# Kernel tuning notes

Hardware: AMD Instinct MI355X
Metric: run time of the kernel (lower is better)

## Reference

```python
import jax, jax.numpy as jnp
import numpy as np

B, DIM = 4096, 768
HEADS, DIM_HEAD = 8, 96
INNER = HEADS * DIM_HEAD  # 768
N_IDS = 751


def setup_inputs() -> dict:
    key = jax.random.key(0)
    k1, k2, k3, k4 = jax.random.split(key, 4)
    x = jax.random.normal(k1, (B, DIM), dtype=jnp.float32)
    labels = jax.random.randint(k2, (B,), 0, N_IDS, dtype=jnp.int64)
    W_qkv = jax.random.normal(k3, (DIM, 3 * INNER), dtype=jnp.float32) * 0.02
    W_out = jax.random.normal(k4, (INNER, DIM), dtype=jnp.float32) * 0.02
    return {"x": x, "labels": labels, "W_qkv": W_qkv, "W_out": W_out}


def reference(x, labels, W_qkv, W_out):
    scale = DIM_HEAD ** -0.5
    qkv = x @ W_qkv  # [b, 3*inner]
    q, k, v = jnp.split(qkv, 3, axis=-1)  # each [b, inner]
    # rearrange 'b (h d) -> h b d'
    split_heads = lambda t: t.reshape(B, HEADS, DIM_HEAD).transpose(1, 0, 2)
    q, k, v = split_heads(q), split_heads(k), split_heads(v)
    dots = jnp.einsum('hid,hjd->hij', q, k) * scale  # [h, b, b]
    attn = jax.nn.softmax(dots, axis=-1)
    # post-softmax pairwise label-equality mask (no renormalization)
    mask = (labels[:, None] == labels[None, :]).astype(attn.dtype)  # [b, b]
    out = jnp.einsum('hij,hjd->hid', attn * mask[None], v)  # [h, b, d]
    out = out.transpose(1, 0, 2).reshape(B, INNER)  # 'h i d -> i (h d)'
    return out @ W_out
```

## Files before the change

### kernel.cpp

```cpp
#include <hip/hip_runtime.h>
#include <hip/hip_bf16.h>

#define BB 4096
#define DIMM 768
#define NHEADS 8
#define DHEAD 96
#define NIDS 751
#define QKSCALE 0.10206207261596577f
#define PVCH 96

typedef _Float16 f16x8 __attribute__((ext_vector_type(8)));
typedef float f32x4 __attribute__((ext_vector_type(4)));

__device__ __forceinline__ void split2(float v, _Float16* hi, _Float16* lo) {
    _Float16 h = (_Float16)v;
    *hi = h;
    *lo = (_Float16)(v - (float)h);
}

__device__ __forceinline__ float rec2(const _Float16* hi, const _Float16* lo, size_t idx) {
    return (float)hi[idx] + (float)lo[idx];
}

__device__ __forceinline__ void gl_lds16(const void* g, void* l) {
    __builtin_amdgcn_global_load_lds(
        (const __attribute__((address_space(1))) unsigned int*)g,
        (__attribute__((address_space(3))) unsigned int*)l, 16, 0, 0);
}

__global__ void k_zero2(float* a, int na, float* b, int nb) {
    int i = blockIdx.x * blockDim.x + threadIdx.x;
    if (i < na) a[i] = 0.0f;
    int j = i - na;
    if (j >= 0 && j < nb) b[j] = 0.0f;
}

__global__ void k_split(const float* __restrict__ in, _Float16* __restrict__ hi,
                        _Float16* __restrict__ lo, float s, int n) {
    int i = blockIdx.x * blockDim.x + threadIdx.x;
    if (i < n) split2(in[i] * s, &hi[i], &lo[i]);
}

__global__ void k_tsplit(const float* __restrict__ W, _Float16* __restrict__ Th,
                         _Float16* __restrict__ Tl, float s, int K, int N) {
    __shared__ float tile[32][33];
    int k0 = blockIdx.y * 32, n0 = blockIdx.x * 32;
    int tx = threadIdx.x, ty = threadIdx.y;
    for (int r = ty; r < 32; r += 8) tile[r][tx] = W[(size_t)(k0 + r) * N + n0 + tx];
    __syncthreads();
    for (int r = ty; r < 32; r += 8) {
        int n = n0 + r, k = k0 + tx;
        split2(tile[tx][r] * s, &Th[(size_t)n * K + k], &Tl[(size_t)n * K + k]);
    }
}

__global__ __launch_bounds__(1024) void k_groups(
    const int* __restrict__ labels, int* __restrict__ perm,
    int* __restrict__ gstart, int* __restrict__ gcnt) {
    __shared__ int cnt[1024], scn[1024], strt[1024], cur[1024];
    int tid = threadIdx.x;
    cnt[tid] = 0; cur[tid] = 0;
    __syncthreads();
    for (int i = tid; i < BB; i += 1024) atomicAdd(&cnt[labels[i]], 1);
    __syncthreads();
    int v = cnt[tid];
    scn[tid] = v;
    __syncthreads();
#pragma unroll
    for (int off = 1; off < 1024; off <<= 1) {
        int t = (tid >= off) ? scn[tid - off] : 0;
        __syncthreads();
        scn[tid] += t;
        __syncthreads();
    }
    int st = scn[tid] - v;
    strt[tid] = st;
    if (tid < NIDS) { gstart[tid] = st; gcnt[tid] = v; }
    __syncthreads();
    for (int i = tid; i < BB; i += 1024) {
        int lb = labels[i];
        int p = strt[lb] + atomicAdd(&cur[lb], 1);
        perm[p] = i;
    }
}

template <int EPI>
__global__ __launch_bounds__(512, 4) void k_gemm(
    const _Float16* __restrict__ Ah, const _Float16* __restrict__ Al, int lda,
    const _Float16* __restrict__ Bh, const _Float16* __restrict__ Bl, int ldb,
    int K, float inv,
    float* __restrict__ outF, _Float16* __restrict__ oh, _Float16* __restrict__ ol) {
    __shared__ __align__(16) _Float16 sAh[2][128 * 32];
    __shared__ __align__(16) _Float16 sAl[2][128 * 32];
    __shared__ __align__(16) _Float16 sBh[2][128 * 32];
    __shared__ __align__(16) _Float16 sBl[2][128 * 32];
    const int tid = threadIdx.x;
    const int lane = tid & 63;
    const int wave = tid >> 6;
    const int wm = wave >> 2, wn = wave & 3;
    unsigned wg = blockIdx.y * gridDim.x + blockIdx.x;
    unsigned nwg = gridDim.x * gridDim.y;
    unsigned swz = ((nwg & 7u) == 0u) ? (wg & 7u) * (nwg >> 3) + (wg >> 3) : wg;
    unsigned by = swz / gridDim.x;
    unsigned bx = swz - by * gridDim.x;
    const int m0 = by * 128, n0 = bx * 128;
    const int kbase = blockIdx.z * K;
    const int srow = tid >> 2;
    const int scol = (tid & 3) * 8;
    const int rl = lane & 15;
    const int g8 = (lane >> 4) * 8;

    const _Float16* gAh0 = Ah + (size_t)(m0 + srow) * lda + kbase + scol;
    const _Float16* gAl0 = Al + (size_t)(m0 + srow) * lda + kbase + scol;
    const _Float16* gBh0 = Bh + (size_t)(n0 + srow) * ldb + kbase + scol;
    const _Float16* gBl0 = Bl + (size_t)(n0 + srow) * ldb + kbase + scol;
    const int d0 = tid * 8;

    auto stage = [&](int b, int kk) {
        gl_lds16(gAh0 + kk, &sAh[b][d0]);
        gl_lds16(gAl0 + kk, &sAl[b][d0]);
        gl_lds16(gBh0 + kk, &sBh[b][d0]);
        gl_lds16(gBl0 + kk, &sBl[b][d0]);
    };

    f32x4 acc[4][2];
    const f32x4 vzero = {0.f, 0.f, 0.f, 0.f};
#pragma unroll
    for (int a = 0; a < 4; a++)
#pragma unroll
        for (int b = 0; b < 2; b++) acc[a][b] = vzero;

    const int KS = K >> 5;
    stage(0, 0);
    for (int ks = 0; ks < KS; ks++) {
        __syncthreads();
        if (ks + 1 < KS) stage((ks + 1) & 1, (ks + 1) << 5);
        const int cb = ks & 1;
        f16x8 ah[4], al[4], bh[2], bl[2];
#pragma unroll
        for (int t = 0; t < 4; t++) {
            ah[t] = *(const f16x8*)&sAh[cb][(wm * 64 + t * 16 + rl) * 32 + g8];
            al[t] = *(const f16x8*)&sAl[cb][(wm * 64 + t * 16 + rl) * 32 + g8];
        }
#pragma unroll
        for (int u = 0; u < 2; u++) {
            bh[u] = *(const f16x8*)&sBh[cb][(wn * 32 + u * 16 + rl) * 32 + g8];
            bl[u] = *(const f16x8*)&sBl[cb][(wn * 32 + u * 16 + rl) * 32 + g8];
        }
#pragma unroll
        for (int a = 0; a < 4; a++)
#pragma unroll
            for (int b = 0; b < 2; b++) {
                acc[a][b] = __builtin_amdgcn_mfma_f32_16x16x32_f16(ah[a], bh[b], acc[a][b], 0, 0, 0);
                acc[a][b] = __builtin_amdgcn_mfma_f32_16x16x32_f16(ah[a], bl[b], acc[a][b], 0, 0, 0);
                acc[a][b] = __builtin_amdgcn_mfma_f32_16x16x32_f16(al[a], bh[b], acc[a][b], 0, 0, 0);
            }
    }

#pragma unroll
    for (int a = 0; a < 4; a++)
#pragma unroll
        for (int b = 0; b < 2; b++) {
            f32x4 d = acc[a][b] * inv;
            int n = n0 + wn * 32 + b * 16 + rl;
            int mb = m0 + wm * 64 + a * 16 + (lane >> 4) * 4;
#pragma unroll
            for (int r = 0; r < 4; r++) {
                int m = mb + r;
                if constexpr (EPI == 0) {
                    if (n < 1536) {
                        split2(d[r] * 16.0f, &oh[(size_t)m * 1536 + n], &ol[(size_t)m * 1536 + n]);
                    } else {
                        outF[(size_t)m * DIMM + (n - 1536)] = d[r];
                    }
                } else {
                    atomicAdd(&outF[(size_t)m * DIMM + n], d[r]);
                }
            }
        }
}

__global__ __launch_bounds__(256) void k_qksum(
    const _Float16* __restrict__ QKh, float* __restrict__ lsum) {
    __shared__ __align__(16) _Float16 sB[2][128 * 104];
    const int tid = threadIdx.x;
    const int lane = tid & 63;
    const int wave = tid >> 6;
    const int wm = wave >> 1, wn = wave & 1;
    unsigned wg = blockIdx.y * gridDim.x + blockIdx.x;
    const int head = (int)(wg & 7u);
    unsigned rest = wg >> 3;
    const int m0 = (int)(rest & 31u) * 128;
    const int nq = (int)(rest >> 5);
    const int cA = head * DHEAD;
    const int cB = DIMM + head * DHEAD;
    const int rl = lane & 15;
    const int g8 = (lane >> 4) * 8;

    f16x8 ah[3][4];
#pragma unroll
    for (int k = 0; k < 3; k++)
#pragma unroll
        for (int a = 0; a < 4; a++)
            ah[k][a] = *(const f16x8*)(QKh +
                (size_t)(m0 + wm * 64 + a * 16 + rl) * 1536 + cA + k * 32 + g8);

    auto stage = [&](int b, int tile) {
        const int n0 = tile * 128;
#pragma unroll
        for (int rd = 0; rd < 7; rd++) {
            int idx = rd * 256 + tid;
            if (idx < 1664) {
                int row = idx / 13;
                int c = idx - row * 13;
                int col = (c < 12) ? c * 8 : 0;
                gl_lds16(QKh + (size_t)(n0 + row) * 1536 + cB + col,
                         &sB[b][idx * 8]);
            }
        }
    };

    const f32x4 vzero = {0.f, 0.f, 0.f, 0.f};
    f32x4 es[4];
#pragma unroll
    for (int a = 0; a < 4; a++) es[a] = vzero;
    const float esc = QKSCALE * (1.0f / 256.0f);

    stage(0, nq * 8);
    for (int nt = 0; nt < 8; nt++) {
        __syncthreads();
        if (nt < 7) stage((nt + 1) & 1, nq * 8 + nt + 1);
        const int cb = nt & 1;
        f32x4 acc[4][4];
#pragma unroll
        for (int a = 0; a < 4; a++)
#pragma unroll
            for (int b = 0; b < 4; b++) acc[a][b] = vzero;
#pragma unroll
        for (int k = 0; k < 3; k++) {
            f16x8 bh[4];
#pragma unroll
            for (int b = 0; b < 4; b++)
                bh[b] = *(const f16x8*)&sB[cb][(wn * 64 + b * 16 + rl) * 104 + k * 32 + g8];
#pragma unroll
            for (int a = 0; a < 4; a++)
#pragma unroll
                for (int b = 0; b < 4; b++)
                    acc[a][b] = __builtin_amdgcn_mfma_f32_16x16x32_f16(ah[k][a], bh[b], acc[a][b], 0, 0, 0);
        }
#pragma unroll
        for (int a = 0; a < 4; a++)
#pragma unroll
            for (int b = 0; b < 4; b++)
#pragma unroll
                for (int r = 0; r < 4; r++)
                    es[a][r] += __expf(acc[a][b][r] * esc);
    }

    float (*red)[33] = (float (*)[33])&sB[0][0];
#pragma unroll
    for (int a = 0; a < 4; a++) {
        int rb = wm * 64 + a * 16 + (lane >> 4) * 4;
#pragma unroll
        for (int r = 0; r < 4; r++) red[rb + r][wn * 16 + rl] = es[a][r];
    }
    __syncthreads();
    if (tid < 128) {
        float s = 0.f;
#pragma unroll
        for (int c = 0; c < 32; c++) s += red[tid][c];
        atomicAdd(&lsum[(size_t)head * BB + m0 + tid], s);
    }
}

__global__ __launch_bounds__(256) void k_pv(
    const _Float16* __restrict__ QKh, const _Float16* __restrict__ QKl,
    const float* __restrict__ vbuf, const float* __restrict__ lsum,
    const int* __restrict__ labels, const int* __restrict__ perm,
    const int* __restrict__ gstart, const int* __restrict__ gcnt,
    _Float16* __restrict__ oh, _Float16* __restrict__ ol) {
    const int i = blockIdx.x;
    const int tid = threadIdx.x;
    const int wave = tid >> 6;
    const int lane = tid & 63;
    __shared__ float wv[NHEADS][PVCH];
    __shared__ int pidx[PVCH];
    const int lab = labels[i];
    const int st = gstart[lab];
    const int cnt = gcnt[lab];
    const float esc = QKSCALE * (1.0f / 256.0f);

    float q0[NHEADS], q1[NHEADS], invl[NHEADS];
#pragma unroll
    for (int h = 0; h < NHEADS; h++) {
        size_t base = (size_t)i * 1536 + h * DHEAD;
        q0[h] = rec2(QKh, QKl, base + lane);
        q1[h] = (lane < 32) ? rec2(QKh, QKl, base + 64 + lane) : 0.0f;
        invl[h] = 1.0f / lsum[(size_t)h * BB + i];
    }
    const int d1 = tid + 256, d2 = tid + 512;
    const int h0 = tid / DHEAD, h1 = d1 / DHEAD, h2 = d2 / DHEAD;
    float acc0 = 0.f, acc1 = 0.f, acc2 = 0.f;

    for (int b0 = 0; b0 < cnt; b0 += PVCH) {
        int ch = cnt - b0; if (ch > PVCH) ch = PVCH;
        __syncthreads();
        if (tid < ch) pidx[tid] = perm[st + b0 + tid];
        __syncthreads();
        for (int t = wave; t < NHEADS * ch; t += 4) {
            int hh = t & 7, jj = t >> 3;
            size_t kb = (size_t)pidx[jj] * 1536 + DIMM + hh * DHEAD;
            float p = q0[hh] * rec2(QKh, QKl, kb + lane);
            if (lane < 32) p += q1[hh] * rec2(QKh, QKl, kb + 64 + lane);
#pragma unroll
            for (int m = 32; m >= 1; m >>= 1) p += __shfl_xor(p, m);
            if (lane == 0) wv[hh][jj] = __expf(p * esc) * invl[hh];
        }
        __syncthreads();
        for (int jj = 0; jj < ch; jj++) {
            const float* vr = vbuf + (size_t)pidx[jj] * DIMM;
            acc0 += wv[h0][jj] * vr[tid];
            acc1 += wv[h1][jj] * vr[d1];
            acc2 += wv[h2][jj] * vr[d2];
        }
    }
    size_t ob = (size_t)i * DIMM;
    split2(acc0 * 16.0f, &oh[ob + tid], &ol[ob + tid]);
    split2(acc1 * 16.0f, &oh[ob + d1], &ol[ob + d1]);
    split2(acc2 * 16.0f, &oh[ob + d2], &ol[ob + d2]);
}

extern "C" void kernel_launch(void* const* d_in, const int* in_sizes, int n_in,
                              void* d_out, int out_size, void* d_ws, size_t ws_size,
                              hipStream_t stream) {
    const float* x = (const float*)d_in[0];
    const int* labels = (const int*)d_in[1];
    const float* Wqkv = (const float*)d_in[2];
    const float* Wout = (const float*)d_in[3];
    float* out = (float*)d_out;

    char* ws = (char*)d_ws;
    size_t off = 0;
    auto alloc = [&](size_t bytes) -> void* {
        void* p = ws + off;
        off += (bytes + 255) & ~(size_t)255;
        return p;
    };
    _Float16* Xh   = (_Float16*)alloc((size_t)BB * DIMM * 2);
    _Float16* Xl   = (_Float16*)alloc((size_t)BB * DIMM * 2);
    _Float16* WqTh = (_Float16*)alloc((size_t)2304 * DIMM * 2);
    _Float16* WqTl = (_Float16*)alloc((size_t)2304 * DIMM * 2);
    _Float16* WoTh = (_Float16*)alloc((size_t)DIMM * DIMM * 2);
    _Float16* WoTl = (_Float16*)alloc((size_t)DIMM * DIMM * 2);
    _Float16* QKh  = (_Float16*)alloc((size_t)BB * 1536 * 2);
    _Float16* QKl  = (_Float16*)alloc((size_t)BB * 1536 * 2);
    float* vbuf    = (float*)alloc((size_t)BB * DIMM * 4);
    float* lsum    = (float*)alloc((size_t)NHEADS * BB * 4);
    _Float16* Oh   = (_Float16*)alloc((size_t)BB * DIMM * 2);
    _Float16* Ol   = (_Float16*)alloc((size_t)BB * DIMM * 2);
    int* perm      = (int*)alloc(BB * 4);
    int* gstart    = (int*)alloc(1024 * 4);
    int* gcnt      = (int*)alloc(1024 * 4);

    const int nz = NHEADS * BB + BB * DIMM;
    k_zero2<<<dim3((nz + 255) / 256), dim3(256), 0, stream>>>(lsum, NHEADS * BB, out, BB * DIMM);
    k_split<<<dim3((BB * DIMM + 255) / 256), dim3(256), 0, stream>>>(x, Xh, Xl, 16.0f, BB * DIMM);
    k_tsplit<<<dim3(2304 / 32, DIMM / 32), dim3(32, 8), 0, stream>>>(Wqkv, WqTh, WqTl, 256.0f, DIMM, 2304);
    k_tsplit<<<dim3(DIMM / 32, DIMM / 32), dim3(32, 8), 0, stream>>>(Wout, WoTh, WoTl, 256.0f, DIMM, DIMM);
    k_groups<<<dim3(1), dim3(1024), 0, stream>>>(labels, perm, gstart, gcnt);

    k_gemm<0><<<dim3(2304 / 128, BB / 128, 1), dim3(512), 0, stream>>>(
        Xh, Xl, DIMM, WqTh, WqTl, DIMM, DIMM, 1.0f / 4096.0f, vbuf, QKh, QKl);
    k_qksum<<<dim3(32, 32), dim3(256), 0, stream>>>(QKh, lsum);
    k_pv<<<dim3(BB), dim3(256), 0, stream>>>(QKh, QKl, vbuf, lsum, labels, perm, gstart, gcnt, Oh, Ol);
    k_gemm<1><<<dim3(DIMM / 128, BB / 128, 2), dim3(512), 0, stream>>>(
        Oh, Ol, DIMM, WoTh, WoTl, DIMM, 384, 1.0f / 4096.0f, out, nullptr, nullptr);
}
```

Before: 312.3 us.

## Batch PV rows per label group, single-buffer GEMMs, raise split-K

k_groups now also builds a work list that splits each label group into chunks of up to 8 rows. k_pv then runs one block per chunk, so each loaded V row is reused across up to 8 query rows instead of being reloaded for every query. The GEMM and QK-sum kernels drop LDS double buffering in favour of a single buffer with extra barriers, aiming for higher occupancy. The output GEMM's split-K factor goes from 2 to 4, which doubles the atomic adds into the output. Losing the prefetch overlap may stall the GEMMs, and MAXENT=1280 assumes the chunk count fits, which holds because there are at most 751+512 chunks.

```diff
diff --git a/kernel.cpp b/kernel.cpp
--- a/kernel.cpp
+++ b/kernel.cpp
@@ -7,7 +7,7 @@
 #define DHEAD 96
 #define NIDS 751
 #define QKSCALE 0.10206207261596577f
-#define PVCH 96
+#define MAXENT 1280
 
 typedef _Float16 f16x8 __attribute__((ext_vector_type(8)));
 typedef float f32x4 __attribute__((ext_vector_type(4)));
@@ -56,7 +56,10 @@
 
 __global__ __launch_bounds__(1024) void k_groups(
     const int* __restrict__ labels, int* __restrict__ perm,
-    int* __restrict__ gstart, int* __restrict__ gcnt) {
+    int* __restrict__ gstart, int* __restrict__ gcnt,
+    int* __restrict__ ent_rs, int* __restrict__ ent_rc,
+    int* __restrict__ ent_st, int* __restrict__ ent_cnt,
+    int* __restrict__ nent) {
     __shared__ int cnt[1024], scn[1024], strt[1024], cur[1024];
     int tid = threadIdx.x;
     cnt[tid] = 0; cur[tid] = 0;
@@ -76,6 +79,28 @@
     int st = scn[tid] - v;
     strt[tid] = st;
     if (tid < NIDS) { gstart[tid] = st; gcnt[tid] = v; }
+    __syncthreads();
+    int ne = (tid < NIDS) ? ((v + 7) >> 3) : 0;
+    scn[tid] = ne;
+    __syncthreads();
+#pragma unroll
+    for (int off = 1; off < 1024; off <<= 1) {
+        int t = (tid >= off) ? scn[tid - off] : 0;
+        __syncthreads();
+        scn[tid] += t;
+        __syncthreads();
+    }
+    int ep = scn[tid] - ne;
+    if (tid == 1023) *nent = scn[1023];
+    if (tid < NIDS) {
+        for (int t = 0; t < ne; t++) {
+            ent_rs[ep + t] = st + t * 8;
+            int rem = v - t * 8;
+            ent_rc[ep + t] = rem < 8 ? rem : 8;
+            ent_st[ep + t] = st;
+            ent_cnt[ep + t] = v;
+        }
+    }
     __syncthreads();
     for (int i = tid; i < BB; i += 1024) {
         int lb = labels[i];
@@ -85,15 +110,15 @@
 }
 
 template <int EPI>
-__global__ __launch_bounds__(512, 4) void k_gemm(
+__global__ __launch_bounds__(512, 8) void k_gemm(
     const _Float16* __restrict__ Ah, const _Float16* __restrict__ Al, int lda,
     const _Float16* __restrict__ Bh, const _Float16* __restrict__ Bl, int ldb,
     int K, float inv,
     float* __restrict__ outF, _Float16* __restrict__ oh, _Float16* __restrict__ ol) {
-    __shared__ __align__(16) _Float16 sAh[2][128 * 32];
-    __shared__ __align__(16) _Float16 sAl[2][128 * 32];
-    __shared__ __align__(16) _Float16 sBh[2][128 * 32];
-    __shared__ __align__(16) _Float16 sBl[2][128 * 32];
+    __shared__ __align__(16) _Float16 sAh[128 * 32];
+    __shared__ __align__(16) _Float16 sAl[128 * 32];
+    __shared__ __align__(16) _Float16 sBh[128 * 32];
+    __shared__ __align__(16) _Float16 sBl[128 * 32];
     const int tid = threadIdx.x;
     const int lane = tid & 63;
     const int wave = tid >> 6;
@@ -116,13 +141,6 @@
     const _Float16* gBl0 = Bl + (size_t)(n0 + srow) * ldb + kbase + scol;
     const int d0 = tid * 8;
 
-    auto stage = [&](int b, int kk) {
-        gl_lds16(gAh0 + kk, &sAh[b][d0]);
-        gl_lds16(gAl0 + kk, &sAl[b][d0]);
-        gl_lds16(gBh0 + kk, &sBh[b][d0]);
-        gl_lds16(gBl0 + kk, &sBl[b][d0]);
-    };
-
     f32x4 acc[4][2];
     const f32x4 vzero = {0.f, 0.f, 0.f, 0.f};
 #pragma unroll
@@ -131,21 +149,25 @@
         for (int b = 0; b < 2; b++) acc[a][b] = vzero;
 
     const int KS = K >> 5;
-    stage(0, 0);
     for (int ks = 0; ks < KS; ks++) {
         __syncthreads();
-        if (ks + 1 < KS) stage((ks + 1) & 1, (ks + 1) << 5);
-        const int cb = ks & 1;
+        const int kk = ks << 5;
+        gl_lds16(gAh0 + kk, &sAh[d0]);
+        gl_lds16(gAl0 + kk, &sAl[d0]);
+        gl_lds16(gBh0 + kk, &sBh[d0]);
+        gl_lds16(gBl0 + kk, &sBl[d0]);
+        __syncthreads();
+
         f16x8 ah[4], al[4], bh[2], bl[2];
 #pragma unroll
         for (int t = 0; t < 4; t++) {
-            ah[t] = *(const f16x8*)&sAh[cb][(wm * 64 + t * 16 + rl) * 32 + g8];
-            al[t] = *(const f16x8*)&sAl[cb][(wm * 64 + t * 16 + rl) * 32 + g8];
+            ah[t] = *(const f16x8*)&sAh[(wm * 64 + t * 16 + rl) * 32 + g8];
+            al[t] = *(const f16x8*)&sAl[(wm * 64 + t * 16 + rl) * 32 + g8];
         }
 #pragma unroll
         for (int u = 0; u < 2; u++) {
-            bh[u] = *(const f16x8*)&sBh[cb][(wn * 32 + u * 16 + rl) * 32 + g8];
-            bl[u] = *(const f16x8*)&sBl[cb][(wn * 32 + u * 16 + rl) * 32 + g8];
+            bh[u] = *(const f16x8*)&sBh[(wn * 32 + u * 16 + rl) * 32 + g8];
+            bl[u] = *(const f16x8*)&sBl[(wn * 32 + u * 16 + rl) * 32 + g8];
         }
 #pragma unroll
         for (int a = 0; a < 4; a++)
@@ -180,9 +202,9 @@
         }
 }
 
-__global__ __launch_bounds__(256) void k_qksum(
+__global__ __launch_bounds__(256, 4) void k_qksum(
     const _Float16* __restrict__ QKh, float* __restrict__ lsum) {
-    __shared__ __align__(16) _Float16 sB[2][128 * 104];
+    __shared__ __align__(16) _Float16 sB[128 * 104];
     const int tid = threadIdx.x;
     const int lane = tid & 63;
     const int wave = tid >> 6;
@@ -205,8 +227,15 @@
             ah[k][a] = *(const f16x8*)(QKh +
                 (size_t)(m0 + wm * 64 + a * 16 + rl) * 1536 + cA + k * 32 + g8);
 
-    auto stage = [&](int b, int tile) {
-        const int n0 = tile * 128;
+    const f32x4 vzero = {0.f, 0.f, 0.f, 0.f};
+    f32x4 es[4];
+#pragma unroll
+    for (int a = 0; a < 4; a++) es[a] = vzero;
+    const float esc = QKSCALE * (1.0f / 256.0f);
+
+    for (int nt = 0; nt < 8; nt++) {
+        __syncthreads();
+        const int n0 = (nq * 8 + nt) * 128;
 #pragma unroll
         for (int rd = 0; rd < 7; rd++) {
             int idx = rd * 256 + tid;
@@ -215,22 +244,11 @@
                 int c = idx - row * 13;
                 int col = (c < 12) ? c * 8 : 0;
                 gl_lds16(QKh + (size_t)(n0 + row) * 1536 + cB + col,
-                         &sB[b][idx * 8]);
+                         &sB[idx * 8]);
             }
         }
-    };
-
-    const f32x4 vzero = {0.f, 0.f, 0.f, 0.f};
-    f32x4 es[4];
-#pragma unroll
-    for (int a = 0; a < 4; a++) es[a] = vzero;
-    const float esc = QKSCALE * (1.0f / 256.0f);
-
-    stage(0, nq * 8);
-    for (int nt = 0; nt < 8; nt++) {
-        __syncthreads();
-        if (nt < 7) stage((nt + 1) & 1, nq * 8 + nt + 1);
-        const int cb = nt & 1;
+        __syncthreads();
+
         f32x4 acc[4][4];
 #pragma unroll
         for (int a = 0; a < 4; a++)
@@ -241,7 +259,7 @@
             f16x8 bh[4];
 #pragma unroll
             for (int b = 0; b < 4; b++)
-                bh[b] = *(const f16x8*)&sB[cb][(wn * 64 + b * 16 + rl) * 104 + k * 32 + g8];
+                bh[b] = *(const f16x8*)&sB[(wn * 64 + b * 16 + rl) * 104 + k * 32 + g8];
 #pragma unroll
             for (int a = 0; a < 4; a++)
 #pragma unroll
@@ -257,7 +275,8 @@
                     es[a][r] += __expf(acc[a][b][r] * esc);
     }
 
-    float (*red)[33] = (float (*)[33])&sB[0][0];
+    __syncthreads();
+    float (*red)[33] = (float (*)[33])&sB[0];
 #pragma unroll
     for (int a = 0; a < 4; a++) {
         int rb = wm * 64 + a * 16 + (lane >> 4) * 4;
@@ -276,58 +295,72 @@
 __global__ __launch_bounds__(256) void k_pv(
     const _Float16* __restrict__ QKh, const _Float16* __restrict__ QKl,
     const float* __restrict__ vbuf, const float* __restrict__ lsum,
-    const int* __restrict__ labels, const int* __restrict__ perm,
-    const int* __restrict__ gstart, const int* __restrict__ gcnt,
+    const int* __restrict__ perm,
+    const int* __restrict__ ent_rs, const int* __restrict__ ent_rc,
+    const int* __restrict__ ent_st, const int* __restrict__ ent_cnt,
+    const int* __restrict__ nent,
     _Float16* __restrict__ oh, _Float16* __restrict__ ol) {
-    const int i = blockIdx.x;
+    const int e = blockIdx.x;
+    if (e >= *nent) return;
+    const int rs = ent_rs[e], rc = ent_rc[e];
+    const int st = ent_st[e], cnt = ent_cnt[e];
     const int tid = threadIdx.x;
     const int wave = tid >> 6;
     const int lane = tid & 63;
-    __shared__ float wv[NHEADS][PVCH];
-    __shared__ int pidx[PVCH];
-    const int lab = labels[i];
-    const int st = gstart[lab];
-    const int cnt = gcnt[lab];
+    __shared__ float wv[8][NHEADS][32];
+    __shared__ int pidx[32];
+    __shared__ int rowi[8];
+    if (tid < rc) rowi[tid] = perm[rs + tid];
     const float esc = QKSCALE * (1.0f / 256.0f);
-
-    float q0[NHEADS], q1[NHEADS], invl[NHEADS];
-#pragma unroll
-    for (int h = 0; h < NHEADS; h++) {
-        size_t base = (size_t)i * 1536 + h * DHEAD;
-        q0[h] = rec2(QKh, QKl, base + lane);
-        q1[h] = (lane < 32) ? rec2(QKh, QKl, base + 64 + lane) : 0.0f;
-        invl[h] = 1.0f / lsum[(size_t)h * BB + i];
-    }
-    const int d1 = tid + 256, d2 = tid + 512;
-    const int h0 = tid / DHEAD, h1 = d1 / DHEAD, h2 = d2 / DHEAD;
-    float acc0 = 0.f, acc1 = 0.f, acc2 = 0.f;
-
-    for (int b0 = 0; b0 < cnt; b0 += PVCH) {
-        int ch = cnt - b0; if (ch > PVCH) ch = PVCH;
-        __syncthreads();
-        if (tid < ch) pidx[tid] = perm[st + b0 + tid];
-        __syncthreads();
-        for (int t = wave; t < NHEADS * ch; t += 4) {
-            int hh = t & 7, jj = t >> 3;
-            size_t kb = (size_t)pidx[jj] * 1536 + DIMM + hh * DHEAD;
-            float p = q0[hh] * rec2(QKh, QKl, kb + lane);
-            if (lane < 32) p += q1[hh] * rec2(QKh, QKl, kb + 64 + lane);
-#pragma unroll
-            for (int m = 32; m >= 1; m >>= 1) p += __shfl_xor(p, m);
-            if (lane == 0) wv[hh][jj] = __expf(p * esc) * invl[hh];
+    const int c1 = tid + 256, c2 = tid + 512;
+    const int h0 = tid / DHEAD, h1 = c1 / DHEAD, h2 = c2 / DHEAD;
+    float a0[8], a1[8], a2[8];
+#pragma unroll
+    for (int ii = 0; ii < 8; ii++) { a0[ii] = 0.f; a1[ii] = 0.f; a2[ii] = 0.f; }
+    __syncthreads();
+
+    for (int jb = 0; jb < cnt; jb += 32) {
+        int ch = cnt - jb; if (ch > 32) ch = 32;
+        __syncthreads();
+        if (tid < ch) pidx[tid] = perm[st + jb + tid];
+        __syncthreads();
+        for (int t = wave; t < rc * NHEADS; t += 4) {
+            int ii = t >> 3, h = t & 7;
+            int i = rowi[ii];
+            size_t qb = (size_t)i * 1536 + h * DHEAD;
+            float q0 = rec2(QKh, QKl, qb + lane);
+            float q1 = (lane < 32) ? rec2(QKh, QKl, qb + 64 + lane) : 0.f;
+            float invl = 1.0f / lsum[(size_t)h * BB + i];
+            for (int jj = 0; jj < ch; jj++) {
+                size_t kb = (size_t)pidx[jj] * 1536 + DIMM + h * DHEAD;
+                float p = q0 * rec2(QKh, QKl, kb + lane);
+                if (lane < 32) p += q1 * rec2(QKh, QKl, kb + 64 + lane);
+#pragma unroll
+                for (int m = 32; m >= 1; m >>= 1) p += __shfl_xor(p, m);
+                if (lane == 0) wv[ii][h][jj] = __expf(p * esc) * invl;
+            }
         }
         __syncthreads();
         for (int jj = 0; jj < ch; jj++) {
             const float* vr = vbuf + (size_t)pidx[jj] * DIMM;
-            acc0 += wv[h0][jj] * vr[tid];
-            acc1 += wv[h1][jj] * vr[d1];
-            acc2 += wv[h2][jj] * vr[d2];
-        }
-    }
-    size_t ob = (size_t)i * DIMM;
-    split2(acc0 * 16.0f, &oh[ob + tid], &ol[ob + tid]);
-    split2(acc1 * 16.0f, &oh[ob + d1], &ol[ob + d1]);
-    split2(acc2 * 16.0f, &oh[ob + d2], &ol[ob + d2]);
+            float v0 = vr[tid], v1 = vr[c1], v2 = vr[c2];
+#pragma unroll
+            for (int ii = 0; ii < 8; ii++) {
+                if (ii >= rc) break;
+                a0[ii] += wv[ii][h0][jj] * v0;
+                a1[ii] += wv[ii][h1][jj] * v1;
+                a2[ii] += wv[ii][h2][jj] * v2;
+            }
+        }
+    }
+#pragma unroll
+    for (int ii = 0; ii < 8; ii++) {
+        if (ii >= rc) break;
+        size_t ob = (size_t)rowi[ii] * DIMM;
+        split2(a0[ii] * 16.0f, &oh[ob + tid], &ol[ob + tid]);
+        split2(a1[ii] * 16.0f, &oh[ob + c1], &ol[ob + c1]);
+        split2(a2[ii] * 16.0f, &oh[ob + c2], &ol[ob + c2]);
+    }
 }
 
 extern "C" void kernel_launch(void* const* d_in, const int* in_sizes, int n_in,
@@ -361,18 +394,25 @@
     int* perm      = (int*)alloc(BB * 4);
     int* gstart    = (int*)alloc(1024 * 4);
     int* gcnt      = (int*)alloc(1024 * 4);
+    int* ent_rs    = (int*)alloc(MAXENT * 4);
+    int* ent_rc    = (int*)alloc(MAXENT * 4);
+    int* ent_st    = (int*)alloc(MAXENT * 4);
+    int* ent_cnt   = (int*)alloc(MAXENT * 4);
+    int* nent      = (int*)alloc(256);
 
     const int nz = NHEADS * BB + BB * DIMM;
     k_zero2<<<dim3((nz + 255) / 256), dim3(256), 0, stream>>>(lsum, NHEADS * BB, out, BB * DIMM);
     k_split<<<dim3((BB * DIMM + 255) / 256), dim3(256), 0, stream>>>(x, Xh, Xl, 16.0f, BB * DIMM);
     k_tsplit<<<dim3(2304 / 32, DIMM / 32), dim3(32, 8), 0, stream>>>(Wqkv, WqTh, WqTl, 256.0f, DIMM, 2304);
     k_tsplit<<<dim3(DIMM / 32, DIMM / 32), dim3(32, 8), 0, stream>>>(Wout, WoTh, WoTl, 256.0f, DIMM, DIMM);
-    k_groups<<<dim3(1), dim3(1024), 0, stream>>>(labels, perm, gstart, gcnt);
+    k_groups<<<dim3(1), dim3(1024), 0, stream>>>(labels, perm, gstart, gcnt,
+                                                 ent_rs, ent_rc, ent_st, ent_cnt, nent);
 
     k_gemm<0><<<dim3(2304 / 128, BB / 128, 1), dim3(512), 0, stream>>>(
         Xh, Xl, DIMM, WqTh, WqTl, DIMM, DIMM, 1.0f / 4096.0f, vbuf, QKh, QKl);
     k_qksum<<<dim3(32, 32), dim3(256), 0, stream>>>(QKh, lsum);
-    k_pv<<<dim3(BB), dim3(256), 0, stream>>>(QKh, QKl, vbuf, lsum, labels, perm, gstart, gcnt, Oh, Ol);
-    k_gemm<1><<<dim3(DIMM / 128, BB / 128, 2), dim3(512), 0, stream>>>(
-        Oh, Ol, DIMM, WoTh, WoTl, DIMM, 384, 1.0f / 4096.0f, out, nullptr, nullptr);
-}
+    k_pv<<<dim3(MAXENT), dim3(256), 0, stream>>>(QKh, QKl, vbuf, lsum, perm,
+                                                 ent_rs, ent_rc, ent_st, ent_cnt, nent, Oh, Ol);
+    k_gemm<1><<<dim3(DIMM / 128, BB / 128, 4), dim3(512), 0, stream>>>(
+        Oh, Ol, DIMM, WoTh, WoTl, DIMM, 192, 1.0f / 4096.0f, out, nullptr, nullptr);
+}
```

Measured after the change: 442.4 us. 41.7% more time.
